# Kernel tuning notes

Hardware: AMD Instinct MI355X
Metric: run time of the kernel (lower is better)

Reference implementation:

```python
import jax, jax.numpy as jnp
import numpy as np

D_MODEL = 192
D_STATE = 16
D_CONV = 4
EXPAND = 2
D_INNER = EXPAND * D_MODEL          # 384
DT_RANK = (D_MODEL + 15) // 16       # 12
B_, C_, DD, HH, WW = 2, 192, 32, 32, 16


def setup_inputs() -> dict:
    key = jax.random.key(0)
    ks = jax.random.split(key, 10)
    s = 0.02
    return {
        "x": jax.random.normal(ks[0], (B_, C_, DD, HH, WW), jnp.float32),
        # Mamba params (mamba-ssm layout)
        "in_proj_w": jax.random.normal(ks[1], (2 * D_INNER, D_MODEL), jnp.float32) * s,
        "conv_w": jax.random.normal(ks[2], (D_INNER, 1, D_CONV), jnp.float32) * s,
        "conv_b": jnp.zeros((D_INNER,), jnp.float32),
        "x_proj_w": jax.random.normal(ks[3], (DT_RANK + 2 * D_STATE, D_INNER), jnp.float32) * s,
        "dt_proj_w": jax.random.normal(ks[4], (D_INNER, DT_RANK), jnp.float32) * s,
        # bias chosen so softplus(dt) is small/positive, as in mamba's dt init
        "dt_proj_b": jax.random.uniform(ks[5], (D_INNER,), jnp.float32, minval=-4.0, maxval=-2.0),
        "A_log": jnp.log(jnp.broadcast_to(jnp.arange(1, D_STATE + 1, dtype=jnp.float32), (D_INNER, D_STATE))),
        "D_param": jnp.ones((D_INNER,), jnp.float32),
        "out_proj_w": jax.random.normal(ks[6], (D_MODEL, D_INNER), jnp.float32) * s,
        # 1x1x1 Conv3d projection (input_dim -> output_dim)
        "proj_w": jax.random.normal(ks[7], (C_, C_), jnp.float32) * s,
        "proj_b": jnp.zeros((C_,), jnp.float32),
    }


def _mamba(xf, in_proj_w, conv_w, conv_b, x_proj_w, dt_proj_w, dt_proj_b, A_log, D_param, out_proj_w):
    # xf: (B, L, d_model)
    B, L, _ = xf.shape
    xz = xf @ in_proj_w.T                          # (B, L, 2*d_inner)
    u, z = jnp.split(xz, 2, axis=-1)               # each (B, L, d_inner)

    # causal depthwise conv1d over L, kernel D_CONV
    uc = jnp.transpose(u, (0, 2, 1))               # (B, d_inner, L)
    up = jnp.pad(uc, ((0, 0), (0, 0), (D_CONV - 1, 0)))
    conv = sum(up[:, :, k:k + L] * conv_w[None, :, 0, k, None] for k in range(D_CONV))
    conv = conv + conv_b[None, :, None]
    u = jax.nn.silu(jnp.transpose(conv, (0, 2, 1)))  # (B, L, d_inner)

    dbl = u @ x_proj_w.T                           # (B, L, dt_rank + 2*d_state)
    dt_low = dbl[..., :DT_RANK]
    Bm = dbl[..., DT_RANK:DT_RANK + D_STATE]       # (B, L, d_state)
    Cm = dbl[..., DT_RANK + D_STATE:]              # (B, L, d_state)
    dt = jax.nn.softplus(dt_low @ dt_proj_w.T + dt_proj_b)  # (B, L, d_inner)

    A = -jnp.exp(A_log)                            # (d_inner, d_state)

    def step(h, inputs):
        u_t, dt_t, B_t, C_t = inputs               # (B,d_inner),(B,d_inner),(B,d_state),(B,d_state)
        dA = jnp.exp(dt_t[..., None] * A)          # (B, d_inner, d_state)
        h = dA * h + dt_t[..., None] * B_t[:, None, :] * u_t[..., None]
        y = jnp.einsum('bds,bs->bd', h, C_t)
        return h, y

    h0 = jnp.zeros((B, D_INNER, D_STATE), xf.dtype)
    xs = (jnp.transpose(u, (1, 0, 2)), jnp.transpose(dt, (1, 0, 2)),
          jnp.transpose(Bm, (1, 0, 2)), jnp.transpose(Cm, (1, 0, 2)))
    _, ys = jax.lax.scan(step, h0, xs)             # ys: (L, B, d_inner)
    y = jnp.transpose(ys, (1, 0, 2)) + u * D_param
    y = y * jax.nn.silu(z)
    return y @ out_proj_w.T                        # (B, L, d_model)


def reference(x, in_proj_w, conv_w, conv_b, x_proj_w, dt_proj_w, dt_proj_b,
              A_log, D_param, out_proj_w, proj_w, proj_b):
    B, C, Dz, H, W = x.shape
    # InstanceNorm3d (affine=False, eps=1e-5, biased variance)
    mu = x.mean(axis=(2, 3, 4), keepdims=True)
    var = x.var(axis=(2, 3, 4), keepdims=True)
    xn = (x - mu) / jnp.sqrt(var + 1e-5)
    L = Dz * H * W
    xf = jnp.transpose(xn.reshape(B, C, L), (0, 2, 1))  # (B, L, C)
    y = _mamba(xf, in_proj_w, conv_w, conv_b, x_proj_w, dt_proj_w, dt_proj_b,
               A_log, D_param, out_proj_w)
    y = jnp.transpose(y, (0, 2, 1)).reshape(B, C, Dz, H, W)
    # 1x1x1 Conv3d projection
    out = jnp.einsum('bcdhw,oc->bodhw', y, proj_w) + proj_b[None, :, None, None, None]
    return out
```

## Files before the change

kernel.cpp:

```cpp
#include <hip/hip_runtime.h>
#include <hip/hip_bf16.h>
#include <math.h>

#define BB   2
#define CM   192
#define DI   384
#define LL   16384
#define NST  16
#define RDT  12
#define XJ   44
#define NC   512
#define CLEN 32
#define NCH  (NC / 16)
#define DBS  64
#define XZS  768
#define CVT  32
#define DTT  32
#define BK   32

typedef __attribute__((ext_vector_type(8))) short bf16x8;
typedef __attribute__((ext_vector_type(4))) float f32x4;
typedef unsigned short ushort_t;

static __device__ __forceinline__ ushort_t f2bf(float f) {
  __hip_bfloat16 h = __float2bfloat16(f);
  return *reinterpret_cast<ushort_t*>(&h);
}
static __device__ __forceinline__ float bf2f(ushort_t u) {
  __hip_bfloat16 h;
  *reinterpret_cast<ushort_t*>(&h) = u;
  return __bfloat162float(h);
}

__global__ __launch_bounds__(256) void fuse_proj_kernel(
    const float* __restrict__ pw, const float* __restrict__ ow, float* __restrict__ PW) {
  int idx = blockIdx.x * 256 + threadIdx.x;
  if (idx >= CM * DI) return;
  int o = idx / DI, d = idx % DI;
  float s = 0.f;
  #pragma unroll 4
  for (int c = 0; c < CM; c++) s += pw[o * CM + c] * ow[c * DI + d];
  PW[idx] = s;
}

__global__ __launch_bounds__(256) void cvt_weights_kernel(
    const float* __restrict__ ipw, const float* __restrict__ xpw,
    const float* __restrict__ PW,
    ushort_t* __restrict__ ipw_bf, ushort_t* __restrict__ xpw_bf,
    ushort_t* __restrict__ PW_bf) {
  int i = blockIdx.x * 256 + threadIdx.x;
  if (i < 2 * DI * CM) ipw_bf[i] = f2bf(ipw[i]);
  if (i < 128 * DI) {
    int r = i / DI;
    xpw_bf[i] = (r < XJ) ? f2bf(xpw[i]) : (ushort_t)0;
  }
  if (i < 256 * DI) {
    int r = i / DI;
    PW_bf[i] = (r < CM) ? f2bf(PW[i]) : (ushort_t)0;
  }
}

__global__ __launch_bounds__(256) void norm_stats_kernel(
    const float* __restrict__ x, float* __restrict__ mu, float* __restrict__ rstd) {
  int bc = blockIdx.x;
  const float* p = x + (size_t)bc * LL;
  float s = 0.f, ss = 0.f;
  for (int i = threadIdx.x * 4; i < LL; i += 256 * 4) {
    float4 v = *(const float4*)(p + i);
    s += v.x + v.y + v.z + v.w;
    ss += v.x * v.x + v.y * v.y + v.z * v.z + v.w * v.w;
  }
  for (int o = 32; o > 0; o >>= 1) {
    s += __shfl_down(s, o, 64);
    ss += __shfl_down(ss, o, 64);
  }
  __shared__ float sb[4], ssb[4];
  int wid = threadIdx.x >> 6;
  if ((threadIdx.x & 63) == 0) { sb[wid] = s; ssb[wid] = ss; }
  __syncthreads();
  if (threadIdx.x == 0) {
    s = sb[0] + sb[1] + sb[2] + sb[3];
    ss = ssb[0] + ssb[1] + ssb[2] + ssb[3];
    float m = s * (1.f / LL);
    float var = ss * (1.f / LL) - m * m;
    mu[bc] = m;
    rstd[bc] = 1.f / sqrtf(var + 1e-5f);
  }
}

__global__ __launch_bounds__(256) void xt_norm_kernel(
    const float* __restrict__ x, const float* __restrict__ mu,
    const float* __restrict__ rstd, ushort_t* __restrict__ xT) {
  __shared__ ushort_t T[64][72];
  int t0 = blockIdx.x * 64, c0 = blockIdx.y * 64, b = blockIdx.z;
  int tid = threadIdx.x;
  int c = tid >> 2, tq = (tid & 3) * 16;
  int bc = b * CM + c0 + c;
  const float* xp = x + (size_t)bc * LL + t0 + tq;
  float m = mu[bc], rs = rstd[bc];
  #pragma unroll
  for (int j = 0; j < 16; j += 4) {
    float4 v = *(const float4*)(xp + j);
    T[c][tq + j + 0] = f2bf((v.x - m) * rs);
    T[c][tq + j + 1] = f2bf((v.y - m) * rs);
    T[c][tq + j + 2] = f2bf((v.z - m) * rs);
    T[c][tq + j + 3] = f2bf((v.w - m) * rs);
  }
  __syncthreads();
  int t = tid >> 2, cq = (tid & 3) * 16;
  unsigned int ob[8];
  #pragma unroll
  for (int j = 0; j < 8; j++)
    ob[j] = (unsigned int)T[cq + 2 * j][t] | ((unsigned int)T[cq + 2 * j + 1][t] << 16);
  ushort_t* op = xT + ((size_t)b * LL + t0 + t) * CM + c0 + cq;
  *(uint4*)(op)     = make_uint4(ob[0], ob[1], ob[2], ob[3]);
  *(uint4*)(op + 8) = make_uint4(ob[4], ob[5], ob[6], ob[7]);
}

template <bool TOUT, typename OutT>
__global__ __launch_bounds__(256) void gemm_lds(
    const ushort_t* __restrict__ A, const ushort_t* __restrict__ BT,
    OutT* __restrict__ C, int K, int Mreal, int MT,
    long strideBT, long strideC, int ldc,
    const float* __restrict__ bias) {
  __shared__ ushort_t Asm[2][128 * BK];
  __shared__ ushort_t Bsm[2][128 * BK];

  int id = blockIdx.x;
  int per = MT * 8;
  int g = id / per, r = id % per;
  int nt = g * 8 + (r & 7);
  int mt = r >> 3;
  int b  = nt >> 7;
  long n0 = (long)(nt & 127) * 128;
  int m0 = mt * 128;

  int tid = threadIdx.x;
  int lane = tid & 63, wave = tid >> 6;
  const ushort_t* Bbase = BT + (size_t)b * strideBT;

  int srow0 = wave * 32 + (lane >> 2);
  int sk = (lane & 3) * 8;

  f32x4 acc[4][4];
  #pragma unroll
  for (int mi = 0; mi < 4; mi++)
    #pragma unroll
    for (int ni = 0; ni < 4; ni++) acc[mi][ni] = (f32x4){0.f, 0.f, 0.f, 0.f};

  int mh = wave & 1, nh = wave >> 1;
  int fr = lane & 15, fk = (lane >> 4) * 8;

  int nsteps = K / BK;
  {
    const ushort_t* As0 = A + (size_t)(m0 + srow0) * K + sk;
    const ushort_t* Bs0 = Bbase + (size_t)(n0 + srow0) * K + sk;
    __builtin_amdgcn_global_load_lds(As0, &Asm[0][wave * 1024], 16, 0, 0);
    __builtin_amdgcn_global_load_lds(As0 + (size_t)16 * K, &Asm[0][wave * 1024 + 512], 16, 0, 0);
    __builtin_amdgcn_global_load_lds(Bs0, &Bsm[0][wave * 1024], 16, 0, 0);
    __builtin_amdgcn_global_load_lds(Bs0 + (size_t)16 * K, &Bsm[0][wave * 1024 + 512], 16, 0, 0);
  }
  __syncthreads();
  int cur = 0;
  for (int s = 0; s < nsteps; s++) {
    if (s + 1 < nsteps) {
      int k0 = (s + 1) * BK;
      const ushort_t* As0 = A + (size_t)(m0 + srow0) * K + k0 + sk;
      const ushort_t* Bs0 = Bbase + (size_t)(n0 + srow0) * K + k0 + sk;
      __builtin_amdgcn_global_load_lds(As0, &Asm[cur ^ 1][wave * 1024], 16, 0, 0);
      __builtin_amdgcn_global_load_lds(As0 + (size_t)16 * K, &Asm[cur ^ 1][wave * 1024 + 512], 16, 0, 0);
      __builtin_amdgcn_global_load_lds(Bs0, &Bsm[cur ^ 1][wave * 1024], 16, 0, 0);
      __builtin_amdgcn_global_load_lds(Bs0 + (size_t)16 * K, &Bsm[cur ^ 1][wave * 1024 + 512], 16, 0, 0);
    }
    bf16x8 fa[4], fb[4];
    #pragma unroll
    for (int mi = 0; mi < 4; mi++)
      fa[mi] = *(const bf16x8*)&Asm[cur][(mh * 64 + mi * 16 + fr) * BK + fk];
    #pragma unroll
    for (int ni = 0; ni < 4; ni++)
      fb[ni] = *(const bf16x8*)&Bsm[cur][(nh * 64 + ni * 16 + fr) * BK + fk];
    #pragma unroll
    for (int mi = 0; mi < 4; mi++)
      #pragma unroll
      for (int ni = 0; ni < 4; ni++) {
        if constexpr (TOUT)
          acc[mi][ni] = __builtin_amdgcn_mfma_f32_16x16x32_bf16(fb[ni], fa[mi], acc[mi][ni], 0, 0, 0);
        else
          acc[mi][ni] = __builtin_amdgcn_mfma_f32_16x16x32_bf16(fa[mi], fb[ni], acc[mi][ni], 0, 0, 0);
      }
    __syncthreads();
    cur ^= 1;
  }

  int cq = (lane >> 4) * 4;
  if constexpr (TOUT) {
    #pragma unroll
    for (int ni = 0; ni < 4; ni++)
      #pragma unroll
      for (int rg = 0; rg < 4; rg++) {
        long n = n0 + nh * 64 + ni * 16 + cq + rg;
        OutT* cp = C + (size_t)b * strideC + n * ldc + m0 + mh * 64 + fr;
        #pragma unroll
        for (int mi = 0; mi < 4; mi++) {
          int mrow = m0 + mh * 64 + mi * 16 + fr;
          if (mrow < Mreal) {
            float v = acc[mi][ni][rg];
            if constexpr (sizeof(OutT) == 2) cp[mi * 16] = f2bf(v);
            else                             cp[mi * 16] = v;
          }
        }
      }
  } else {
    #pragma unroll
    for (int mi = 0; mi < 4; mi++)
      #pragma unroll
      for (int rg = 0; rg < 4; rg++) {
        int m = m0 + mh * 64 + mi * 16 + cq + rg;
        if (m < Mreal) {
          float bv = bias ? bias[m] : 0.f;
          OutT* cp = C + (size_t)b * strideC + (size_t)m * ldc + n0 + nh * 64 + fr;
          #pragma unroll
          for (int ni = 0; ni < 4; ni++)
            cp[ni * 16] = acc[mi][ni][rg] + bv;
        }
      }
  }
}

__global__ __launch_bounds__(384) void conv_silu_kernel(
    const ushort_t* __restrict__ xzT, const float* __restrict__ conv_w,
    const float* __restrict__ conv_b, ushort_t* __restrict__ u_t) {
  __shared__ ushort_t Us[CVT + 3][DI];
  int t0 = blockIdx.x * CVT;
  int b = blockIdx.y;
  int tid = threadIdx.x;
  #pragma unroll
  for (int r = 0; r < CVT + 3; r++) {
    int t = t0 - 3 + r;
    Us[r][tid] = (t >= 0) ? xzT[((size_t)b * LL + t) * XZS + tid] : (ushort_t)0;
  }
  float w0 = conv_w[tid * 4 + 0], w1 = conv_w[tid * 4 + 1];
  float w2 = conv_w[tid * 4 + 2], w3 = conv_w[tid * 4 + 3];
  float cb = conv_b[tid];
  __syncthreads();
  ushort_t* up = u_t + ((size_t)b * LL + t0) * DI + tid;
  float xm3 = bf2f(Us[0][tid]);
  float xm2 = bf2f(Us[1][tid]);
  float xm1 = bf2f(Us[2][tid]);
  #pragma unroll
  for (int t = 0; t < CVT; t++) {
    float xc = bf2f(Us[t + 3][tid]);
    float a = cb + w3 * xc + w2 * xm1 + w1 * xm2 + w0 * xm3;
    float sv = a / (1.f + __expf(-a));
    up[(size_t)t * DI] = f2bf(sv);
    xm3 = xm2; xm2 = xm1; xm1 = xc;
  }
}

__global__ __launch_bounds__(384) void dt_kernel(
    const float* __restrict__ dblT, const float* __restrict__ dtw,
    const float* __restrict__ dtb, float* __restrict__ dt_t) {
  __shared__ float Ls[DTT * 12];
  int t0 = blockIdx.x * DTT;
  int b = blockIdx.y;
  int tid = threadIdx.x;
  if (tid < DTT * 12) {
    int t = tid / 12, rr = tid - t * 12;
    Ls[tid] = dblT[((size_t)b * LL + t0 + t) * DBS + rr];
  }
  float dw[12];
  #pragma unroll
  for (int rr = 0; rr < 12; rr += 4)
    *(float4*)(dw + rr) = *(const float4*)(dtw + tid * 12 + rr);
  float db = dtb[tid];
  __syncthreads();
  float* op = dt_t + ((size_t)b * LL + t0) * DI + tid;
  #pragma unroll
  for (int t = 0; t < DTT; t++) {
    float acc = db;
    #pragma unroll
    for (int rr = 0; rr < 12; rr++) acc = fmaf(Ls[t * 12 + rr], dw[rr], acc);
    float v = (acc > 15.f) ? acc : __logf(1.f + __expf(acc));
    op[(size_t)t * DI] = v;
  }
}

__global__ __launch_bounds__(384) void scan_phase1(
    const float* __restrict__ dt_t, const ushort_t* __restrict__ u_t,
    const float* __restrict__ dblT, const float* __restrict__ A_log,
    float* __restrict__ hend, float* __restrict__ Pbuf) {
  int tid = threadIdx.x;
  int chunk = blockIdx.x, b = blockIdx.y;
  int t0 = chunk * CLEN;
  const float* dblB = dblT + ((size_t)b * LL + t0) * DBS + RDT;
  int d = tid;
  int bd = b * DI + d;
  float av0 = -expf(A_log[d * NST]);
  float av_[NST];
  bool ok = true;
  #pragma unroll
  for (int j = 0; j < NST; j++) {
    av_[j] = -expf(A_log[d * NST + j]);
    ok = ok && (fabsf(av_[j] - av0 * (float)(j + 1)) <= 1e-4f * fabsf(av_[j]));
  }
  const float* dtp = dt_t + ((size_t)b * LL + t0) * DI + d;
  const ushort_t* up = u_t + ((size_t)b * LL + t0) * DI + d;
  float h[NST];
  #pragma unroll
  for (int j = 0; j < NST; j++) h[j] = 0.f;

  size_t o = ((size_t)bd * NC + chunk) * NST;
  if (__all(ok)) {
    float W = 1.f;
    #pragma unroll 2
    for (int t = 0; t < CLEN; t++) {
      float dtv = dtp[(size_t)t * DI];
      float uv  = bf2f(up[(size_t)t * DI]);
      float4 B0 = *(const float4*)(dblB + t * DBS + 0);
      float4 B1 = *(const float4*)(dblB + t * DBS + 4);
      float4 B2 = *(const float4*)(dblB + t * DBS + 8);
      float4 B3 = *(const float4*)(dblB + t * DBS + 12);
      float q = dtv * uv;
      float p1 = __expf(dtv * av0);
      W *= p1;
      float p2 = p1 * p1, p4 = p2 * p2, p8 = p4 * p4;
      float p3 = p2 * p1, p5 = p4 * p1, p6 = p4 * p2, p7 = p4 * p3;
      h[0]  = fmaf(p1, h[0],  q * B0.x);
      h[1]  = fmaf(p2, h[1],  q * B0.y);
      h[2]  = fmaf(p3, h[2],  q * B0.z);
      h[3]  = fmaf(p4, h[3],  q * B0.w);
      h[4]  = fmaf(p5, h[4],  q * B1.x);
      h[5]  = fmaf(p6, h[5],  q * B1.y);
      h[6]  = fmaf(p7, h[6],  q * B1.z);
      h[7]  = fmaf(p8, h[7],  q * B1.w);
      h[8]  = fmaf(p8 * p1, h[8],  q * B2.x);
      h[9]  = fmaf(p8 * p2, h[9],  q * B2.y);
      h[10] = fmaf(p8 * p3, h[10], q * B2.z);
      h[11] = fmaf(p8 * p4, h[11], q * B2.w);
      h[12] = fmaf(p8 * p5, h[12], q * B3.x);
      h[13] = fmaf(p8 * p6, h[13], q * B3.y);
      h[14] = fmaf(p8 * p7, h[14], q * B3.z);
      h[15] = fmaf(p8 * p8, h[15], q * B3.w);
    }
    #pragma unroll
    for (int j = 0; j < NST; j += 4)
      *(float4*)(hend + o + j) = make_float4(h[j], h[j+1], h[j+2], h[j+3]);
    float P[NST];
    float pj = W;
    #pragma unroll
    for (int j = 0; j < NST; j++) { P[j] = pj; pj *= W; }
    #pragma unroll
    for (int j = 0; j < NST; j += 4)
      *(float4*)(Pbuf + o + j) = make_float4(P[j], P[j+1], P[j+2], P[j+3]);
  } else {
    float S = 0.f;
    for (int t = 0; t < CLEN; t++) {
      float dtv = dtp[(size_t)t * DI];
      float uv  = bf2f(up[(size_t)t * DI]);
      float q = dtv * uv;
      S += dtv;
      #pragma unroll
      for (int j = 0; j < NST; j++)
        h[j] = __expf(dtv * av_[j]) * h[j] + q * dblB[t * DBS + j];
    }
    #pragma unroll
    for (int j = 0; j < NST; j++) {
      hend[o + j] = h[j];
      Pbuf[o + j] = __expf(S * av_[j]);
    }
  }
}

__global__ __launch_bounds__(256) void scan_combine(
    float* __restrict__ hend, const float* __restrict__ Pbuf) {
  __shared__ float sP[16][16], sH[16][16];
  int bd = blockIdx.x;
  int s = threadIdx.x & 15, g = threadIdx.x >> 4;
  size_t base = ((size_t)bd * NC + g * NCH) * NST + s;
  float Pl = 1.f, Hl = 0.f;
  #pragma unroll
  for (int k = 0; k < NCH; k++) {
    size_t o = base + (size_t)k * NST;
    float p = Pbuf[o], he = hend[o];
    Hl = fmaf(p, Hl, he);
    Pl *= p;
  }
  sP[g][s] = Pl; sH[g][s] = Hl;
  __syncthreads();
  if (threadIdx.x < 16) {
    int ss = threadIdx.x;
    float c = 0.f;
    #pragma unroll
    for (int gg = 0; gg < 16; gg++) {
      float tmp = sH[gg][ss];
      float pp  = sP[gg][ss];
      sH[gg][ss] = c;
      c = fmaf(pp, c, tmp);
    }
  }
  __syncthreads();
  float c = sH[g][s];
  #pragma unroll
  for (int k = 0; k < NCH; k++) {
    size_t o = base + (size_t)k * NST;
    float p = Pbuf[o], he = hend[o];
    hend[o] = c;
    c = fmaf(p, c, he);
  }
}

__global__ __launch_bounds__(384) void scan_phase3(
    const float* __restrict__ dt_t, const ushort_t* __restrict__ u_t,
    const float* __restrict__ dblT, const float* __restrict__ A_log,
    const float* __restrict__ hin, const float* __restrict__ Dp,
    const ushort_t* __restrict__ xzT, ushort_t* __restrict__ ym_t) {
  int tid = threadIdx.x;
  int chunk = blockIdx.x, b = blockIdx.y;
  int t0 = chunk * CLEN;
  const float* dblB = dblT + ((size_t)b * LL + t0) * DBS + RDT;
  int d = tid;
  int bd = b * DI + d;
  float av0 = -expf(A_log[d * NST]);
  float av_[NST];
  bool ok = true;
  #pragma unroll
  for (int j = 0; j < NST; j++) {
    av_[j] = -expf(A_log[d * NST + j]);
    ok = ok && (fabsf(av_[j] - av0 * (float)(j + 1)) <= 1e-4f * fabsf(av_[j]));
  }
  const float* dtp = dt_t + ((size_t)b * LL + t0) * DI + d;
  const ushort_t* up = u_t + ((size_t)b * LL + t0) * DI + d;
  const ushort_t* zp = xzT + ((size_t)b * LL + t0) * XZS + DI + d;
  ushort_t* ymp = ym_t + ((size_t)b * LL + t0) * DI + d;

  float h[NST];
  const float* hi = hin + ((size_t)bd * NC + chunk) * NST;
  #pragma unroll
  for (int j = 0; j < NST; j += 4) {
    float4 v = *(const float4*)(hi + j);
    h[j] = v.x; h[j+1] = v.y; h[j+2] = v.z; h[j+3] = v.w;
  }
  float Dv = Dp[d];

  if (__all(ok)) {
    #pragma unroll 2
    for (int t = 0; t < CLEN; t++) {
      float dtv = dtp[(size_t)t * DI];
      float uv  = bf2f(up[(size_t)t * DI]);
      float zv  = bf2f(zp[(size_t)t * XZS]);
      float4 B0 = *(const float4*)(dblB + t * DBS + 0);
      float4 B1 = *(const float4*)(dblB + t * DBS + 4);
      float4 B2 = *(const float4*)(dblB + t * DBS + 8);
      float4 B3 = *(const float4*)(dblB + t * DBS + 12);
      float4 C0 = *(const float4*)(dblB + t * DBS + 16);
      float4 C1 = *(const float4*)(dblB + t * DBS + 20);
      float4 C2 = *(const float4*)(dblB + t * DBS + 24);
      float4 C3 = *(const float4*)(dblB + t * DBS + 28);
      float q = dtv * uv;
      float p1 = __expf(dtv * av0);
      float p2 = p1 * p1, p4 = p2 * p2, p8 = p4 * p4;
      float p3 = p2 * p1, p5 = p4 * p1, p6 = p4 * p2, p7 = p4 * p3;
      float y0, y1, y2, y3;
      h[0]  = fmaf(p1, h[0],  q * B0.x); y0 = h[0] * C0.x;
      h[1]  = fmaf(p2, h[1],  q * B0.y); y1 = h[1] * C0.y;
      h[2]  = fmaf(p3, h[2],  q * B0.z); y2 = h[2] * C0.z;
      h[3]  = fmaf(p4, h[3],  q * B0.w); y3 = h[3] * C0.w;
      h[4]  = fmaf(p5, h[4],  q * B1.x); y0 = fmaf(h[4],  C1.x, y0);
      h[5]  = fmaf(p6, h[5],  q * B1.y); y1 = fmaf(h[5],  C1.y, y1);
      h[6]  = fmaf(p7, h[6],  q * B1.z); y2 = fmaf(h[6],  C1.z, y2);
      h[7]  = fmaf(p8, h[7],  q * B1.w); y3 = fmaf(h[7],  C1.w, y3);
      h[8]  = fmaf(p8 * p1, h[8],  q * B2.x); y0 = fmaf(h[8],  C2.x, y0);
      h[9]  = fmaf(p8 * p2, h[9],  q * B2.y); y1 = fmaf(h[9],  C2.y, y1);
      h[10] = fmaf(p8 * p3, h[10], q * B2.z); y2 = fmaf(h[10], C2.z, y2);
      h[11] = fmaf(p8 * p4, h[11], q * B2.w); y3 = fmaf(h[11], C2.w, y3);
      h[12] = fmaf(p8 * p5, h[12], q * B3.x); y0 = fmaf(h[12], C3.x, y0);
      h[13] = fmaf(p8 * p6, h[13], q * B3.y); y1 = fmaf(h[13], C3.y, y1);
      h[14] = fmaf(p8 * p7, h[14], q * B3.z); y2 = fmaf(h[14], C3.z, y2);
      h[15] = fmaf(p8 * p8, h[15], q * B3.w); y3 = fmaf(h[15], C3.w, y3);
      float y = (y0 + y1) + (y2 + y3);
      float yv = (y + uv * Dv) * (zv / (1.f + __expf(-zv)));
      ymp[(size_t)t * DI] = f2bf(yv);
    }
  } else {
    for (int t = 0; t < CLEN; t++) {
      float dtv = dtp[(size_t)t * DI];
      float uv  = bf2f(up[(size_t)t * DI]);
      float zv  = bf2f(zp[(size_t)t * XZS]);
      float q = dtv * uv;
      float y = 0.f;
      #pragma unroll
      for (int j = 0; j < NST; j++) {
        h[j] = __expf(dtv * av_[j]) * h[j] + q * dblB[t * DBS + j];
        y = fmaf(h[j], dblB[t * DBS + NST + j], y);
      }
      float yv = (y + uv * Dv) * (zv / (1.f + __expf(-zv)));
      ymp[(size_t)t * DI] = f2bf(yv);
    }
  }
}

extern "C" void kernel_launch(void* const* d_in, const int* in_sizes, int n_in,
                              void* d_out, int out_size, void* d_ws, size_t ws_size,
                              hipStream_t stream) {
  const float* x         = (const float*)d_in[0];
  const float* in_proj_w = (const float*)d_in[1];
  const float* conv_w    = (const float*)d_in[2];
  const float* conv_b    = (const float*)d_in[3];
  const float* x_proj_w  = (const float*)d_in[4];
  const float* dt_proj_w = (const float*)d_in[5];
  const float* dt_proj_b = (const float*)d_in[6];
  const float* A_log     = (const float*)d_in[7];
  const float* D_param   = (const float*)d_in[8];
  const float* out_proj_w= (const float*)d_in[9];
  const float* proj_w    = (const float*)d_in[10];
  const float* proj_b    = (const float*)d_in[11];
  float* out = (float*)d_out;

  float* w = (float*)d_ws;
  float*    mu     = w;
  float*    rstd   = w + 512;
  float*    PW     = w + 1024;
  ushort_t* PW_bf  = (ushort_t*)(w + 74752);
  ushort_t* ipw_bf = (ushort_t*)(w + 123904);
  ushort_t* xpw_bf = (ushort_t*)(w + 197632);
  ushort_t* xT     = (ushort_t*)(w + 222208);
  ushort_t* xzT    = (ushort_t*)(w + 3367936);
  ushort_t* u_t    = (ushort_t*)(w + 15950848);
  float*    dblT   = w + 22242304;
  float*    dt_t   = w + 24339456;
  ushort_t* ym_t   = (ushort_t*)(w + 36922368);
  float*    hend   = w + 43213824;
  float*    Pbuf   = w + 49505280;
  size_t need = 55796736;
  if (ws_size < need * sizeof(float)) return;

  norm_stats_kernel<<<dim3(BB * CM), dim3(256), 0, stream>>>(x, mu, rstd);
  fuse_proj_kernel<<<dim3((CM * DI + 255) / 256), dim3(256), 0, stream>>>(proj_w, out_proj_w, PW);
  cvt_weights_kernel<<<dim3((2 * DI * CM + 255) / 256), dim3(256), 0, stream>>>(
      in_proj_w, x_proj_w, PW, ipw_bf, xpw_bf, PW_bf);
  xt_norm_kernel<<<dim3(LL / 64, CM / 64, BB), dim3(256), 0, stream>>>(x, mu, rstd, xT);

  gemm_lds<true, ushort_t><<<dim3(256 * 6), dim3(256), 0, stream>>>(
      ipw_bf, xT, xzT, CM, 768, 6, (long)LL * CM, (long)LL * XZS, XZS, nullptr);

  conv_silu_kernel<<<dim3(LL / CVT, BB), dim3(384), 0, stream>>>(xzT, conv_w, conv_b, u_t);

  gemm_lds<true, float><<<dim3(256 * 1), dim3(256), 0, stream>>>(
      xpw_bf, u_t, dblT, DI, 64, 1, (long)LL * DI, (long)LL * DBS, DBS, nullptr);

  dt_kernel<<<dim3(LL / DTT, BB), dim3(384), 0, stream>>>(dblT, dt_proj_w, dt_proj_b, dt_t);

  scan_phase1<<<dim3(NC, BB), dim3(384), 0, stream>>>(dt_t, u_t, dblT, A_log, hend, Pbuf);
  scan_combine<<<dim3(BB * DI), dim3(256), 0, stream>>>(hend, Pbuf);
  scan_phase3<<<dim3(NC, BB), dim3(384), 0, stream>>>(dt_t, u_t, dblT, A_log, hend, D_param, xzT, ym_t);

  gemm_lds<false, float><<<dim3(256 * 2), dim3(256), 0, stream>>>(
      PW_bf, ym_t, out, DI, CM, 2, (long)LL * DI, (long)CM * LL, LL, proj_b);
}
```

Baseline: 226.8 us.

## Fuse dt projection and softplus into scan phases; store chunk dt sums instead of decay products

Removes the standalone dt_kernel and its 2x16384x384 fp32 dt buffer. Both scan phases now recompute dt from the low-rank dbl columns with a 12-term dot product plus softplus on every timestep. Phase 1 writes only the per-chunk sum of dt, not 16 decay products, and scan_combine rebuilds the decays with exp(S*A). This cuts global memory traffic and one launch, at the cost of duplicated dt arithmetic in phase 1 and phase 3 and extra exps in the combine.

```diff
diff --git a/kernel.cpp b/kernel.cpp
--- a/kernel.cpp
+++ b/kernel.cpp
@@ -15,7 +15,6 @@
 #define DBS  64
 #define XZS  768
 #define CVT  32
-#define DTT  32
 #define BK   32
 
 typedef __attribute__((ext_vector_type(8))) short bf16x8;
@@ -257,42 +256,15 @@
   }
 }
 
-__global__ __launch_bounds__(384) void dt_kernel(
-    const float* __restrict__ dblT, const float* __restrict__ dtw,
-    const float* __restrict__ dtb, float* __restrict__ dt_t) {
-  __shared__ float Ls[DTT * 12];
-  int t0 = blockIdx.x * DTT;
-  int b = blockIdx.y;
-  int tid = threadIdx.x;
-  if (tid < DTT * 12) {
-    int t = tid / 12, rr = tid - t * 12;
-    Ls[tid] = dblT[((size_t)b * LL + t0 + t) * DBS + rr];
-  }
-  float dw[12];
-  #pragma unroll
-  for (int rr = 0; rr < 12; rr += 4)
-    *(float4*)(dw + rr) = *(const float4*)(dtw + tid * 12 + rr);
-  float db = dtb[tid];
-  __syncthreads();
-  float* op = dt_t + ((size_t)b * LL + t0) * DI + tid;
-  #pragma unroll
-  for (int t = 0; t < DTT; t++) {
-    float acc = db;
-    #pragma unroll
-    for (int rr = 0; rr < 12; rr++) acc = fmaf(Ls[t * 12 + rr], dw[rr], acc);
-    float v = (acc > 15.f) ? acc : __logf(1.f + __expf(acc));
-    op[(size_t)t * DI] = v;
-  }
-}
-
 __global__ __launch_bounds__(384) void scan_phase1(
-    const float* __restrict__ dt_t, const ushort_t* __restrict__ u_t,
-    const float* __restrict__ dblT, const float* __restrict__ A_log,
-    float* __restrict__ hend, float* __restrict__ Pbuf) {
+    const ushort_t* __restrict__ u_t, const float* __restrict__ dblT,
+    const float* __restrict__ A_log,
+    const float* __restrict__ dtw, const float* __restrict__ dtb,
+    float* __restrict__ hend, float* __restrict__ Sbuf) {
   int tid = threadIdx.x;
   int chunk = blockIdx.x, b = blockIdx.y;
   int t0 = chunk * CLEN;
-  const float* dblB = dblT + ((size_t)b * LL + t0) * DBS + RDT;
+  const float* dblB = dblT + ((size_t)b * LL + t0) * DBS;
   int d = tid;
   int bd = b * DI + d;
   float av0 = -expf(A_log[d * NST]);
@@ -303,26 +275,40 @@
     av_[j] = -expf(A_log[d * NST + j]);
     ok = ok && (fabsf(av_[j] - av0 * (float)(j + 1)) <= 1e-4f * fabsf(av_[j]));
   }
-  const float* dtp = dt_t + ((size_t)b * LL + t0) * DI + d;
+  float w12[12];
+  #pragma unroll
+  for (int rr = 0; rr < 12; rr += 4)
+    *(float4*)(w12 + rr) = *(const float4*)(dtw + d * 12 + rr);
+  float db = dtb[d];
   const ushort_t* up = u_t + ((size_t)b * LL + t0) * DI + d;
   float h[NST];
   #pragma unroll
   for (int j = 0; j < NST; j++) h[j] = 0.f;
+  float S = 0.f;
 
   size_t o = ((size_t)bd * NC + chunk) * NST;
   if (__all(ok)) {
-    float W = 1.f;
     #pragma unroll 2
     for (int t = 0; t < CLEN; t++) {
-      float dtv = dtp[(size_t)t * DI];
+      float4 L0 = *(const float4*)(dblB + t * DBS + 0);
+      float4 L1 = *(const float4*)(dblB + t * DBS + 4);
+      float4 L2 = *(const float4*)(dblB + t * DBS + 8);
+      float4 B0 = *(const float4*)(dblB + t * DBS + RDT + 0);
+      float4 B1 = *(const float4*)(dblB + t * DBS + RDT + 4);
+      float4 B2 = *(const float4*)(dblB + t * DBS + RDT + 8);
+      float4 B3 = *(const float4*)(dblB + t * DBS + RDT + 12);
+      float acc = db;
+      acc = fmaf(L0.x, w12[0], acc); acc = fmaf(L0.y, w12[1], acc);
+      acc = fmaf(L0.z, w12[2], acc); acc = fmaf(L0.w, w12[3], acc);
+      acc = fmaf(L1.x, w12[4], acc); acc = fmaf(L1.y, w12[5], acc);
+      acc = fmaf(L1.z, w12[6], acc); acc = fmaf(L1.w, w12[7], acc);
+      acc = fmaf(L2.x, w12[8], acc); acc = fmaf(L2.y, w12[9], acc);
+      acc = fmaf(L2.z, w12[10], acc); acc = fmaf(L2.w, w12[11], acc);
+      float dtv = (acc > 15.f) ? acc : __logf(1.f + __expf(acc));
       float uv  = bf2f(up[(size_t)t * DI]);
-      float4 B0 = *(const float4*)(dblB + t * DBS + 0);
-      float4 B1 = *(const float4*)(dblB + t * DBS + 4);
-      float4 B2 = *(const float4*)(dblB + t * DBS + 8);
-      float4 B3 = *(const float4*)(dblB + t * DBS + 12);
       float q = dtv * uv;
+      S += dtv;
       float p1 = __expf(dtv * av0);
-      W *= p1;
       float p2 = p1 * p1, p4 = p2 * p2, p8 = p4 * p4;
       float p3 = p2 * p1, p5 = p4 * p1, p6 = p4 * p2, p7 = p4 * p3;
       h[0]  = fmaf(p1, h[0],  q * B0.x);
@@ -342,47 +328,41 @@
       h[14] = fmaf(p8 * p7, h[14], q * B3.z);
       h[15] = fmaf(p8 * p8, h[15], q * B3.w);
     }
-    #pragma unroll
-    for (int j = 0; j < NST; j += 4)
-      *(float4*)(hend + o + j) = make_float4(h[j], h[j+1], h[j+2], h[j+3]);
-    float P[NST];
-    float pj = W;
-    #pragma unroll
-    for (int j = 0; j < NST; j++) { P[j] = pj; pj *= W; }
-    #pragma unroll
-    for (int j = 0; j < NST; j += 4)
-      *(float4*)(Pbuf + o + j) = make_float4(P[j], P[j+1], P[j+2], P[j+3]);
   } else {
-    float S = 0.f;
     for (int t = 0; t < CLEN; t++) {
-      float dtv = dtp[(size_t)t * DI];
+      float acc = db;
+      #pragma unroll
+      for (int rr = 0; rr < 12; rr++) acc = fmaf(dblB[t * DBS + rr], w12[rr], acc);
+      float dtv = (acc > 15.f) ? acc : __logf(1.f + __expf(acc));
       float uv  = bf2f(up[(size_t)t * DI]);
       float q = dtv * uv;
       S += dtv;
       #pragma unroll
       for (int j = 0; j < NST; j++)
-        h[j] = __expf(dtv * av_[j]) * h[j] + q * dblB[t * DBS + j];
+        h[j] = __expf(dtv * av_[j]) * h[j] + q * dblB[t * DBS + RDT + j];
     }
-    #pragma unroll
-    for (int j = 0; j < NST; j++) {
-      hend[o + j] = h[j];
-      Pbuf[o + j] = __expf(S * av_[j]);
-    }
-  }
+  }
+  #pragma unroll
+  for (int j = 0; j < NST; j += 4)
+    *(float4*)(hend + o + j) = make_float4(h[j], h[j+1], h[j+2], h[j+3]);
+  Sbuf[(size_t)bd * NC + chunk] = S;
 }
 
 __global__ __launch_bounds__(256) void scan_combine(
-    float* __restrict__ hend, const float* __restrict__ Pbuf) {
+    float* __restrict__ hend, const float* __restrict__ Sbuf,
+    const float* __restrict__ A_log) {
   __shared__ float sP[16][16], sH[16][16];
   int bd = blockIdx.x;
+  int d = bd % DI;
   int s = threadIdx.x & 15, g = threadIdx.x >> 4;
+  float av = -expf(A_log[d * NST + s]);
+  size_t baseS = (size_t)bd * NC + g * NCH;
   size_t base = ((size_t)bd * NC + g * NCH) * NST + s;
   float Pl = 1.f, Hl = 0.f;
   #pragma unroll
   for (int k = 0; k < NCH; k++) {
-    size_t o = base + (size_t)k * NST;
-    float p = Pbuf[o], he = hend[o];
-    Hl = fmaf(p, Hl, he);
+    float p = __expf(Sbuf[baseS + k] * av);
+    Hl = fmaf(p, Hl, hend[base + (size_t)k * NST]);
     Pl *= p;
   }
   sP[g][s] = Pl; sH[g][s] = Hl;
@@ -403,21 +383,23 @@
   #pragma unroll
   for (int k = 0; k < NCH; k++) {
     size_t o = base + (size_t)k * NST;
-    float p = Pbuf[o], he = hend[o];
+    float p = __expf(Sbuf[baseS + k] * av);
+    float he = hend[o];
     hend[o] = c;
     c = fmaf(p, c, he);
   }
 }
 
 __global__ __launch_bounds__(384) void scan_phase3(
-    const float* __restrict__ dt_t, const ushort_t* __restrict__ u_t,
-    const float* __restrict__ dblT, const float* __restrict__ A_log,
+    const ushort_t* __restrict__ u_t, const float* __restrict__ dblT,
+    const float* __restrict__ A_log,
+    const float* __restrict__ dtw, const float* __restrict__ dtb,
     const float* __restrict__ hin, const float* __restrict__ Dp,
     const ushort_t* __restrict__ xzT, ushort_t* __restrict__ ym_t) {
   int tid = threadIdx.x;
   int chunk = blockIdx.x, b = blockIdx.y;
   int t0 = chunk * CLEN;
-  const float* dblB = dblT + ((size_t)b * LL + t0) * DBS + RDT;
+  const float* dblB = dblT + ((size_t)b * LL + t0) * DBS;
   int d = tid;
   int bd = b * DI + d;
   float av0 = -expf(A_log[d * NST]);
@@ -428,7 +410,11 @@
     av_[j] = -expf(A_log[d * NST + j]);
     ok = ok && (fabsf(av_[j] - av0 * (float)(j + 1)) <= 1e-4f * fabsf(av_[j]));
   }
-  const float* dtp = dt_t + ((size_t)b * LL + t0) * DI + d;
+  float w12[12];
+  #pragma unroll
+  for (int rr = 0; rr < 12; rr += 4)
+    *(float4*)(w12 + rr) = *(const float4*)(dtw + d * 12 + rr);
+  float db = dtb[d];
   const ushort_t* up = u_t + ((size_t)b * LL + t0) * DI + d;
   const ushort_t* zp = xzT + ((size_t)b * LL + t0) * XZS + DI + d;
   ushort_t* ymp = ym_t + ((size_t)b * LL + t0) * DI + d;
@@ -445,17 +431,27 @@
   if (__all(ok)) {
     #pragma unroll 2
     for (int t = 0; t < CLEN; t++) {
-      float dtv = dtp[(size_t)t * DI];
+      float4 L0 = *(const float4*)(dblB + t * DBS + 0);
+      float4 L1 = *(const float4*)(dblB + t * DBS + 4);
+      float4 L2 = *(const float4*)(dblB + t * DBS + 8);
+      float4 B0 = *(const float4*)(dblB + t * DBS + RDT + 0);
+      float4 B1 = *(const float4*)(dblB + t * DBS + RDT + 4);
+      float4 B2 = *(const float4*)(dblB + t * DBS + RDT + 8);
+      float4 B3 = *(const float4*)(dblB + t * DBS + RDT + 12);
+      float4 C0 = *(const float4*)(dblB + t * DBS + RDT + 16);
+      float4 C1 = *(const float4*)(dblB + t * DBS + RDT + 20);
+      float4 C2 = *(const float4*)(dblB + t * DBS + RDT + 24);
+      float4 C3 = *(const float4*)(dblB + t * DBS + RDT + 28);
+      float acc = db;
+      acc = fmaf(L0.x, w12[0], acc); acc = fmaf(L0.y, w12[1], acc);
+      acc = fmaf(L0.z, w12[2], acc); acc = fmaf(L0.w, w12[3], acc);
+      acc = fmaf(L1.x, w12[4], acc); acc = fmaf(L1.y, w12[5], acc);
+      acc = fmaf(L1.z, w12[6], acc); acc = fmaf(L1.w, w12[7], acc);
+      acc = fmaf(L2.x, w12[8], acc); acc = fmaf(L2.y, w12[9], acc);
+      acc = fmaf(L2.z, w12[10], acc); acc = fmaf(L2.w, w12[11], acc);
+      float dtv = (acc > 15.f) ? acc : __logf(1.f + __expf(acc));
       float uv  = bf2f(up[(size_t)t * DI]);
       float zv  = bf2f(zp[(size_t)t * XZS]);
-      float4 B0 = *(const float4*)(dblB + t * DBS + 0);
-      float4 B1 = *(const float4*)(dblB + t * DBS + 4);
-      float4 B2 = *(const float4*)(dblB + t * DBS + 8);
-      float4 B3 = *(const float4*)(dblB + t * DBS + 12);
-      float4 C0 = *(const float4*)(dblB + t * DBS + 16);
-      float4 C1 = *(const float4*)(dblB + t * DBS + 20);
-      float4 C2 = *(const float4*)(dblB + t * DBS + 24);
-      float4 C3 = *(const float4*)(dblB + t * DBS + 28);
       float q = dtv * uv;
       float p1 = __expf(dtv * av0);
       float p2 = p1 * p1, p4 = p2 * p2, p8 = p4 * p4;
@@ -483,15 +479,18 @@
     }
   } else {
     for (int t = 0; t < CLEN; t++) {
-      float dtv = dtp[(size_t)t * DI];
+      float acc = db;
+      #pragma unroll
+      for (int rr = 0; rr < 12; rr++) acc = fmaf(dblB[t * DBS + rr], w12[rr], acc);
+      float dtv = (acc > 15.f) ? acc : __logf(1.f + __expf(acc));
       float uv  = bf2f(up[(size_t)t * DI]);
       float zv  = bf2f(zp[(size_t)t * XZS]);
       float q = dtv * uv;
       float y = 0.f;
       #pragma unroll
       for (int j = 0; j < NST; j++) {
-        h[j] = __expf(dtv * av_[j]) * h[j] + q * dblB[t * DBS + j];
-        y = fmaf(h[j], dblB[t * DBS + NST + j], y);
+        h[j] = __expf(dtv * av_[j]) * h[j] + q * dblB[t * DBS + RDT + j];
+        y = fmaf(h[j], dblB[t * DBS + RDT + NST + j], y);
       }
       float yv = (y + uv * Dv) * (zv / (1.f + __expf(-zv)));
       ymp[(size_t)t * DI] = f2bf(yv);
@@ -527,11 +526,10 @@
   ushort_t* xzT    = (ushort_t*)(w + 3367936);
   ushort_t* u_t    = (ushort_t*)(w + 15950848);
   float*    dblT   = w + 22242304;
-  float*    dt_t   = w + 24339456;
-  ushort_t* ym_t   = (ushort_t*)(w + 36922368);
-  float*    hend   = w + 43213824;
-  float*    Pbuf   = w + 49505280;
-  size_t need = 55796736;
+  ushort_t* ym_t   = (ushort_t*)(w + 24339456);
+  float*    hend   = w + 30630912;
+  float*    Sbuf   = w + 36922368;
+  size_t need = 37315584;
   if (ws_size < need * sizeof(float)) return;
 
   norm_stats_kernel<<<dim3(BB * CM), dim3(256), 0, stream>>>(x, mu, rstd);
@@ -548,11 +546,11 @@
   gemm_lds<true, float><<<dim3(256 * 1), dim3(256), 0, stream>>>(
       xpw_bf, u_t, dblT, DI, 64, 1, (long)LL * DI, (long)LL * DBS, DBS, nullptr);
 
-  dt_kernel<<<dim3(LL / DTT, BB), dim3(384), 0, stream>>>(dblT, dt_proj_w, dt_proj_b, dt_t);
-
-  scan_phase1<<<dim3(NC, BB), dim3(384), 0, stream>>>(dt_t, u_t, dblT, A_log, hend, Pbuf);
-  scan_combine<<<dim3(BB * DI), dim3(256), 0, stream>>>(hend, Pbuf);
-  scan_phase3<<<dim3(NC, BB), dim3(384), 0, stream>>>(dt_t, u_t, dblT, A_log, hend, D_param, xzT, ym_t);
+  scan_phase1<<<dim3(NC, BB), dim3(384), 0, stream>>>(
+      u_t, dblT, A_log, dt_proj_w, dt_proj_b, hend, Sbuf);
+  scan_combine<<<dim3(BB * DI), dim3(256), 0, stream>>>(hend, Sbuf, A_log);
+  scan_phase3<<<dim3(NC, BB), dim3(384), 0, stream>>>(
+      u_t, dblT, A_log, dt_proj_w, dt_proj_b, hend, D_param, xzT, ym_t);
 
   gemm_lds<false, float><<<dim3(256 * 2), dim3(256), 0, stream>>>(
       PW_bf, ym_t, out, DI, CM, 2, (long)LL * DI, (long)CM * LL, LL, proj_b);
```

Result: faster. 200.9 us (-11.4%).
